# Kernel tuning notes

Hardware: AMD Instinct MI355X
Metric: run time of the kernel (lower is better)

The kernel has to match this reference:

```python
import jax, jax.numpy as jnp
import numpy as np

B, H, S, D = 1, 16, 4096, 64


def setup_inputs() -> dict:
    key = jax.random.key(0)
    kq, kk, kv = jax.random.split(key, 3)
    Q = jax.random.normal(kq, (B, H, S, D), dtype=jnp.float32)
    K = jax.random.normal(kk, (B, H, S, D), dtype=jnp.float32)
    V = jax.random.normal(kv, (B, H, S, D), dtype=jnp.float32)
    # causal mask, broadcast over batch/heads: True = attend
    mask = jnp.tril(jnp.ones((S, S), dtype=bool))[None, None, :, :]
    return {"Q": Q, "K": K, "V": V, "mask": mask}


def reference(Q, K, V, mask):
    d_k = Q.shape[-1]
    scale = 1.0 / jnp.sqrt(jnp.asarray(d_k, dtype=Q.dtype))
    # [..., q, k] scores; mask==False positions set to -inf before softmax
    scores = jnp.einsum('...qd,...kd->...qk', Q, K) * scale
    scores = jnp.where(mask, scores, jnp.asarray(-jnp.inf, dtype=scores.dtype))
    attn = jax.nn.softmax(scores, axis=-1)
    return jnp.einsum('...qk,...kd->...qd', attn, V)
```

## Files before the change

### kernel.cpp

```cpp
#include <hip/hip_runtime.h>
#include <hip/hip_bf16.h>

typedef __attribute__((ext_vector_type(8))) short short8;
typedef __attribute__((ext_vector_type(4))) short s4v;
typedef __attribute__((ext_vector_type(2))) int   int2v;
typedef __attribute__((ext_vector_type(4))) float floatx4;

#define MFMA16(A,B,C) __builtin_amdgcn_mfma_f32_16x16x32_bf16(A,B,C,0,0,0)
#define LDS_FENCE() asm volatile("s_waitcnt lgkmcnt(0)" ::: "memory")

__device__ __forceinline__ short bf16bits(float x) {
    __hip_bfloat16 h = __float2bfloat16(x);
    return *(short*)&h;
}
__device__ __forceinline__ short8 cvt8(const float* p) {
    floatx4 a = *(const floatx4*)p;
    floatx4 b = *(const floatx4*)(p + 4);
    short8 r;
    r[0]=bf16bits(a.x); r[1]=bf16bits(a.y); r[2]=bf16bits(a.z); r[3]=bf16bits(a.w);
    r[4]=bf16bits(b.x); r[5]=bf16bits(b.y); r[6]=bf16bits(b.z); r[7]=bf16bits(b.w);
    return r;
}
__device__ __forceinline__ short8 cvt8s(const float* p) {
    constexpr float SCL2 = 0.125f * 1.44269504088896f;
    floatx4 a = *(const floatx4*)p;
    floatx4 b = *(const floatx4*)(p + 4);
    a *= SCL2; b *= SCL2;
    short8 r;
    r[0]=bf16bits(a.x); r[1]=bf16bits(a.y); r[2]=bf16bits(a.z); r[3]=bf16bits(a.w);
    r[4]=bf16bits(b.x); r[5]=bf16bits(b.y); r[6]=bf16bits(b.z); r[7]=bf16bits(b.w);
    return r;
}
__device__ __forceinline__ int pk2(float lo, float hi) {
    int r;
    asm("v_cvt_pk_bf16_f32 %0, %1, %2" : "=v"(r) : "v"(lo), "v"(hi));
    return r;
}

__global__ __launch_bounds__(256) void prep(const float* __restrict__ V,
                                            short* __restrict__ VT,
                                            const float* __restrict__ K,
                                            short* __restrict__ K16, int doK)
{
    __shared__ short tile[64 * 65];
    const int t  = threadIdx.x;
    const int h  = blockIdx.x >> 6;
    const int s0 = (blockIdx.x & 63) << 6;
    const float* src = V + ((size_t)h * 4096 + s0) * 64;
    const int r = t >> 4, dq = (t & 15) * 4;
#pragma unroll
    for (int pass = 0; pass < 4; ++pass) {
        const int s = pass * 16 + r;
        floatx4 f = *(const floatx4*)(src + s * 64 + dq);
        short* w = tile + s * 65 + dq;
        w[0] = bf16bits(f.x); w[1] = bf16bits(f.y);
        w[2] = bf16bits(f.z); w[3] = bf16bits(f.w);
    }
    __syncthreads();
    const int d = t >> 2, sc = (t & 3) * 16;
    short8 a, b;
#pragma unroll
    for (int j = 0; j < 8; ++j) a[j] = tile[(sc + j) * 65 + d];
#pragma unroll
    for (int j = 0; j < 8; ++j) b[j] = tile[(sc + 8 + j) * 65 + d];
    short* dst = VT + ((size_t)h * 64 + d) * 4096 + s0 + sc;
    *(short8*)dst       = a;
    *(short8*)(dst + 8) = b;
    if (doK) {
        const size_t base = (size_t)blockIdx.x * 4096 + (size_t)t * 16;
        *(short8*)(K16 + base)     = cvt8(K + base);
        *(short8*)(K16 + base + 8) = cvt8(K + base + 8);
    }
}

template<bool KB16>
__global__ __launch_bounds__(256, 4)
void attn_fast(const float* __restrict__ Qg, const float* __restrict__ Kg,
               const short* __restrict__ K16g, const short* __restrict__ VTg,
               float* __restrict__ Og)
{
    constexpr int S = 4096, D = 64;

    __shared__ __align__(16) short lK[4096];
    __shared__ __align__(16) short lV[4096];
    __shared__ __align__(16) short lP[4096];

    const int tid = threadIdx.x;
    const int wv  = tid >> 6;
    const int ln  = tid & 63;
    const int ll  = ln & 15;
    const int qd  = ln >> 4;

    const int c = blockIdx.x & 255;
    const int s = blockIdx.x >> 8;
    const int h = c & 15;
    const int x = c >> 4;
    const int qblk = (s == 0) ? (63 - x) : (s == 1) ? (32 + x) : (s == 2) ? (31 - x) : x;
    const int qb   = qblk << 6;
    const int qrow = qb + wv * 16;

    const float* Qh  = Qg  + (size_t)h * S * D;
    const float* Kf  = Kg  + (size_t)h * S * D;
    const short* K16 = K16g + (size_t)h * S * D;
    const short* Vt  = VTg + (size_t)h * 64 * S;

    short8 qf0, qf1;
    {
        const float* qp = Qh + (qrow + ll) * D + qd * 8;
        qf0 = cvt8s(qp);
        qf1 = cvt8s(qp + 32);
    }

    floatx4 o[4], ol;
#pragma unroll
    for (int dt = 0; dt < 4; ++dt) o[dt] = (floatx4){0.f, 0.f, 0.f, 0.f};
    ol = (floatx4){0.f, 0.f, 0.f, 0.f};

    short8 ones;
#pragma unroll
    for (int j = 0; j < 8; ++j) ones[j] = (short)0x3F80;

    const int kkey = tid >> 3, kd8 = tid & 7;
    const int koct = kd8 & 3;
    short* kdst = lK + ((kkey >> 4) * 2 + (kd8 >> 2)) * 512
                     + ((((kkey & 15) | (koct << 4)) ^ (koct * 5)) * 8);
    const float* ksrcf = Kf  + kkey * 64 + kd8 * 8;
    const short* ksrc6 = K16 + kkey * 64 + kd8 * 8;
    const int vd = tid >> 2, voct = tid & 3;
    short* vdst = lV + (vd >> 4) * 512
                     + ((((vd & 15) | (voct << 4)) ^ (voct * 5)) * 8);
    const short* vsrc = Vt + (size_t)vd * S + voct * 8;
    const int rblk = ((ll | (qd << 4)) ^ (qd * 5));
    const int pswz  = (ll >> 1) & 3;
    short* lPw = lP + wv * 1024;
    const int pw0 = ll * 32 + (((qd >> 1) ^ pswz) * 8) + (qd & 1) * 4;
    const int prd = ll * 32 + ((qd ^ pswz) * 8);

    const int kv_end = qb + 64;
    const int wv_end = qrow + 16;

    auto ldK = [&](int kv) -> short8 {
        return KB16 ? *(const short8*)(ksrc6 + kv * 64) : cvt8(ksrcf + kv * 64);
    };

    short8 kpre0 = ldK(0),  kpre1 = ldK(32);
    short8 vpre0 = *(const short8*)(vsrc);
    short8 vpre1 = *(const short8*)(vsrc + 32);

    for (int kv = 0; kv < kv_end; kv += 64) {
        __syncthreads();
        *(short8*)kdst          = kpre0;
        *(short8*)(kdst + 2048) = kpre1;
        *(short8*)vdst          = vpre0;
        *(short8*)(vdst + 2048) = vpre1;
        __syncthreads();
        if (kv + 64 < kv_end) {
            kpre0 = ldK(kv + 64);
            kpre1 = ldK(kv + 96);
            vpre0 = *(const short8*)(vsrc + kv + 64);
            vpre1 = *(const short8*)(vsrc + kv + 96);
        }

        if (kv < wv_end) {
            const bool h1 = (kv + 32 < wv_end);
            floatx4 sc0 = (floatx4){0.f, 0.f, 0.f, 0.f};
            floatx4 sc1 = sc0, sc2 = sc0, sc3 = sc0;
            short8 kf;
            __builtin_amdgcn_s_setprio(1);
            kf = ((const short8*)(lK +    0))[rblk]; sc0 = MFMA16(kf, qf0, sc0);
            kf = ((const short8*)(lK +  512))[rblk]; sc0 = MFMA16(kf, qf1, sc0);
            kf = ((const short8*)(lK + 1024))[rblk]; sc1 = MFMA16(kf, qf0, sc1);
            kf = ((const short8*)(lK + 1536))[rblk]; sc1 = MFMA16(kf, qf1, sc1);
            if (h1) {
                kf = ((const short8*)(lK + 2048))[rblk]; sc2 = MFMA16(kf, qf0, sc2);
                kf = ((const short8*)(lK + 2560))[rblk]; sc2 = MFMA16(kf, qf1, sc2);
                kf = ((const short8*)(lK + 3072))[rblk]; sc3 = MFMA16(kf, qf0, sc3);
                kf = ((const short8*)(lK + 3584))[rblk]; sc3 = MFMA16(kf, qf1, sc3);
            }
            __builtin_amdgcn_s_setprio(0);

            float p0[4], p1[4];
#pragma unroll
            for (int r = 0; r < 4; ++r) {
                p0[r] = exp2f(sc0[r]);
                p1[r] = exp2f(sc1[r]);
            }
            if (kv + 31 > qrow) {
                const int qg = qrow + ll;
                const int k0 = kv + qd * 4, k1 = k0 + 16;
#pragma unroll
                for (int r = 0; r < 4; ++r) {
                    if (k0 + r > qg) p0[r] = 0.f;
                    if (k1 + r > qg) p1[r] = 0.f;
                }
            }
            *(int2v*)(lPw + pw0)        = (int2v){pk2(p0[0],p0[1]), pk2(p0[2],p0[3])};
            *(int2v*)(lPw + (pw0 ^ 16)) = (int2v){pk2(p1[0],p1[1]), pk2(p1[2],p1[3])};
            if (h1) {
                float p2[4], p3[4];
#pragma unroll
                for (int r = 0; r < 4; ++r) {
                    p2[r] = exp2f(sc2[r]);
                    p3[r] = exp2f(sc3[r]);
                }
                if (kv + 63 > qrow) {
                    const int qg = qrow + ll;
                    const int k2 = kv + 32 + qd * 4, k3 = k2 + 16;
#pragma unroll
                    for (int r = 0; r < 4; ++r) {
                        if (k2 + r > qg) p2[r] = 0.f;
                        if (k3 + r > qg) p3[r] = 0.f;
                    }
                }
                *(int2v*)(lPw + 512 + pw0)        = (int2v){pk2(p2[0],p2[1]), pk2(p2[2],p2[3])};
                *(int2v*)(lPw + 512 + (pw0 ^ 16)) = (int2v){pk2(p3[0],p3[1]), pk2(p3[2],p3[3])};
            }
            LDS_FENCE();
            short8 pf0 = *(const short8*)(lPw + prd);
            __builtin_amdgcn_s_setprio(1);
#pragma unroll
            for (int dt = 0; dt < 4; ++dt) {
                short8 vf = ((const short8*)(lV + dt * 512))[rblk];
                o[dt] = MFMA16(pf0, vf, o[dt]);
            }
            ol = MFMA16(pf0, ones, ol);
            if (h1) {
                short8 pf1 = *(const short8*)(lPw + 512 + prd);
#pragma unroll
                for (int dt = 0; dt < 4; ++dt) {
                    short8 vf = ((const short8*)(lV + 2048 + dt * 512))[rblk];
                    o[dt] = MFMA16(pf1, vf, o[dt]);
                }
                ol = MFMA16(pf1, ones, ol);
            }
            __builtin_amdgcn_s_setprio(0);
        }
    }

#pragma unroll
    for (int r = 0; r < 4; ++r) {
        const float rl = 1.f / fmaxf(ol[r], 1e-37f);
        const int q = qrow + qd * 4 + r;
        float* op = Og + ((size_t)h * S + q) * D + ll;
#pragma unroll
        for (int dt = 0; dt < 4; ++dt)
            op[dt * 16] = o[dt][r] * rl;
    }
}

__global__ __launch_bounds__(256, 4)
void attn_legacy(const float* __restrict__ Qg, const float* __restrict__ Kg,
                 const float* __restrict__ Vg, float* __restrict__ Og)
{
    constexpr int S = 4096, D = 64;
    constexpr float SCL2 = 0.125f * 1.44269504088896f;
    constexpr float NEG  = -1.0e30f;
    __shared__ __align__(16) short lK[2048];
    __shared__ __align__(16) short lV[2048];
    __shared__ __align__(16) short lP[2048];
    const int tid = threadIdx.x, wv = tid >> 6, ln = tid & 63, ll = ln & 15, qd = ln >> 4;
    const int bid = blockIdx.x, h = bid & 15, qblk = 63 - (bid >> 4), qb = qblk << 6;
    const float* Qh = Qg + (size_t)h * S * D;
    const float* Kh = Kg + (size_t)h * S * D;
    const float* Vh = Vg + (size_t)h * S * D;
    const int qrow = qb + wv * 16;
    short8 qf0, qf1;
    { const float* qp = Qh + (qrow + ll) * D + qd * 8; qf0 = cvt8(qp); qf1 = cvt8(qp + 32); }
    floatx4 o[4]; float mi[4], li[4];
#pragma unroll
    for (int dt = 0; dt < 4; ++dt) o[dt] = (floatx4){0.f,0.f,0.f,0.f};
#pragma unroll
    for (int r = 0; r < 4; ++r) { mi[r] = NEG; li[r] = 0.f; }
    const int k_st = tid >> 3, dbase = (tid & 7) * 8;
    const int sq = (dbase >> 3) & 3, sks = dbase >> 5;
    const int kw_slot = (((k_st >> 4) * 2 + sks) * 64)
                      + (((sq << 4) | (k_st & 15)) ^ (sq | (sks << 2)));
    const int kr0 = ln ^ qd, kr1 = ln ^ (qd | 4), vbit3 = (ln >> 3) & 1;
    const int kv_end = qb + 64, wv_end = qrow + 16;
    for (int kv = 0; kv < kv_end; kv += 32) {
        __syncthreads();
        {
            short8 kval = cvt8(Kh + (kv + k_st) * D + dbase);
            ((short8*)lK)[kw_slot] = kval;
            short8 vval = cvt8(Vh + (kv + k_st) * D + dbase);
            const int vq = (k_st >> 3) << 4, vj = k_st & 7;
#pragma unroll
            for (int i = 0; i < 8; ++i) {
                int d = dbase + i, dt = d >> 4, l2 = d & 15;
                int lp = (vq | l2) ^ (((l2 >> 3) & 1) | (dt << 1));
                lV[dt * 512 + lp * 8 + vj] = vval[i];
            }
        }
        __syncthreads();
        if (kv < wv_end) {
            floatx4 sc0 = (floatx4){0.f,0.f,0.f,0.f}, sc1 = sc0; short8 kf;
            kf = ((const short8*)lK)[0*64+kr0]; sc0 = MFMA16(qf0, kf, sc0);
            kf = ((const short8*)lK)[1*64+kr1]; sc0 = MFMA16(qf1, kf, sc0);
            kf = ((const short8*)lK)[2*64+kr0]; sc1 = MFMA16(qf0, kf, sc1);
            kf = ((const short8*)lK)[3*64+kr1]; sc1 = MFMA16(qf1, kf, sc1);
            float p0[4], p1[4]; const int qg = qrow + qd * 4;
#pragma unroll
            for (int r = 0; r < 4; ++r) { p0[r] = sc0[r]*SCL2; p1[r] = sc1[r]*SCL2; }
            if (kv + 31 > qrow) {
                const int k0 = kv + ll, k1 = kv + 16 + ll;
#pragma unroll
                for (int r = 0; r < 4; ++r) {
                    if (k0 > qg + r) p0[r] = NEG;
                    if (k1 > qg + r) p1[r] = NEG;
                }
            }
#pragma unroll
            for (int r = 0; r < 4; ++r) {
                float mx = fmaxf(p0[r], p1[r]);
                mx = fmaxf(mx, __shfl_xor(mx,1)); mx = fmaxf(mx, __shfl_xor(mx,2));
                mx = fmaxf(mx, __shfl_xor(mx,4)); mx = fmaxf(mx, __shfl_xor(mx,8));
                const float nm = fmaxf(mi[r], mx);
                const float a = exp2f(mi[r] - nm); mi[r] = nm;
                p0[r] = exp2f(p0[r] - nm); p1[r] = exp2f(p1[r] - nm);
                float ps = p0[r] + p1[r];
                ps += __shfl_xor(ps,1); ps += __shfl_xor(ps,2);
                ps += __shfl_xor(ps,4); ps += __shfl_xor(ps,8);
                li[r] = li[r] * a + ps;
#pragma unroll
                for (int dt = 0; dt < 4; ++dt) o[dt][r] *= a;
            }
            {
                const int pbase = wv * 512 + (ll & 7);
                const int dl0 = ((ll >> 3) << 4) + qd * 4;
#pragma unroll
                for (int r = 0; r < 4; ++r) {
                    lP[pbase + (dl0 + r) * 8]      = bf16bits(p0[r]);
                    lP[pbase + (dl0 + 32 + r) * 8] = bf16bits(p1[r]);
                }
            }
            __threadfence_block();
            short8 pf = ((const short8*)lP)[wv * 64 + ln];
#pragma unroll
            for (int dt = 0; dt < 4; ++dt) {
                short8 vf = ((const short8*)lV)[dt * 64 + (ln ^ (vbit3 | (dt << 1)))];
                o[dt] = MFMA16(pf, vf, o[dt]);
            }
        }
    }
#pragma unroll
    for (int r = 0; r < 4; ++r) {
        const float rl = 1.f / fmaxf(li[r], 1e-30f);
        const int q = qrow + qd * 4 + r;
        float* op = Og + ((size_t)h * S + q) * D + ll;
#pragma unroll
        for (int dt = 0; dt < 4; ++dt) op[dt * 16] = o[dt][r] * rl;
    }
}

extern "C" void kernel_launch(void* const* d_in, const int* in_sizes, int n_in,
                              void* d_out, int out_size, void* d_ws, size_t ws_size,
                              hipStream_t stream) {
    const float* Q = (const float*)d_in[0];
    const float* K = (const float*)d_in[1];
    const float* V = (const float*)d_in[2];
    float* O = (float*)d_out;
    const size_t elems  = (size_t)16 * 4096 * 64;
    const size_t oneBuf = elems * sizeof(short);
    if (ws_size >= 2 * oneBuf) {
        short* VT  = (short*)d_ws;
        short* K16 = (short*)d_ws + elems;
        prep<<<dim3(1024), dim3(256), 0, stream>>>(V, VT, K, K16, 1);
        attn_fast<true><<<dim3(1024), dim3(256), 0, stream>>>(Q, K, K16, VT, O);
    } else if (ws_size >= oneBuf) {
        short* VT = (short*)d_ws;
        prep<<<dim3(1024), dim3(256), 0, stream>>>(V, VT, K, VT, 0);
        attn_fast<false><<<dim3(1024), dim3(256), 0, stream>>>(Q, K, nullptr, VT, O);
    } else {
        attn_legacy<<<dim3(1024), dim3(256), 0, stream>>>(Q, K, V, O);
    }
}
```

Measured before the change: 197.7 us.

## Double query rows per wave to reuse K/V LDS fragments across two tiles

Each wave now handles 32 query rows (two 16-row MFMA tiles) instead of 16, so every K and V fragment read from LDS feeds two MFMAs. Blocks cover 128 queries, the grid halves to 512 blocks, and the causal scheduling pairs blocks as (31-x, x) to balance work. The P buffer doubles and launch bounds drop to 2 blocks per CU to leave room for the extra registers. The cost is lower occupancy, fewer blocks to spread across CUs, and more wasted masked work on diagonal tiles.

After: 223.8 us. 1.13x slower.

```diff
diff --git a/kernel.cpp b/kernel.cpp
--- a/kernel.cpp
+++ b/kernel.cpp
@@ -74,7 +74,7 @@
 }
 
 template<bool KB16>
-__global__ __launch_bounds__(256, 4)
+__global__ __launch_bounds__(256, 2)
 void attn_fast(const float* __restrict__ Qg, const float* __restrict__ Kg,
                const short* __restrict__ K16g, const short* __restrict__ VTg,
                float* __restrict__ Og)
@@ -83,7 +83,7 @@
 
     __shared__ __align__(16) short lK[4096];
     __shared__ __align__(16) short lV[4096];
-    __shared__ __align__(16) short lP[4096];
+    __shared__ __align__(16) short lP[8192];
 
     const int tid = threadIdx.x;
     const int wv  = tid >> 6;
@@ -95,26 +95,28 @@
     const int s = blockIdx.x >> 8;
     const int h = c & 15;
     const int x = c >> 4;
-    const int qblk = (s == 0) ? (63 - x) : (s == 1) ? (32 + x) : (s == 2) ? (31 - x) : x;
-    const int qb   = qblk << 6;
-    const int qrow = qb + wv * 16;
+    const int qblk = (s == 0) ? (31 - x) : x;
+    const int qb   = qblk << 7;
+    const int qrow = qb + wv * 32;
 
     const float* Qh  = Qg  + (size_t)h * S * D;
     const float* Kf  = Kg  + (size_t)h * S * D;
     const short* K16 = K16g + (size_t)h * S * D;
     const short* Vt  = VTg + (size_t)h * 64 * S;
 
-    short8 qf0, qf1;
+    short8 qA0, qA1, qB0, qB1;
     {
         const float* qp = Qh + (qrow + ll) * D + qd * 8;
-        qf0 = cvt8s(qp);
-        qf1 = cvt8s(qp + 32);
-    }
-
-    floatx4 o[4], ol;
-#pragma unroll
-    for (int dt = 0; dt < 4; ++dt) o[dt] = (floatx4){0.f, 0.f, 0.f, 0.f};
-    ol = (floatx4){0.f, 0.f, 0.f, 0.f};
+        qA0 = cvt8s(qp);       qA1 = cvt8s(qp + 32);
+        const float* qp2 = qp + 16 * D;
+        qB0 = cvt8s(qp2);      qB1 = cvt8s(qp2 + 32);
+    }
+
+    floatx4 oA[4], oB[4], olA, olB;
+#pragma unroll
+    for (int dt = 0; dt < 4; ++dt) { oA[dt] = (floatx4){0.f,0.f,0.f,0.f}; oB[dt] = oA[dt]; }
+    olA = (floatx4){0.f,0.f,0.f,0.f};
+    olB = olA;
 
     short8 ones;
 #pragma unroll
@@ -132,12 +134,12 @@
     const short* vsrc = Vt + (size_t)vd * S + voct * 8;
     const int rblk = ((ll | (qd << 4)) ^ (qd * 5));
     const int pswz  = (ll >> 1) & 3;
-    short* lPw = lP + wv * 1024;
+    short* lPw = lP + wv * 2048;
     const int pw0 = ll * 32 + (((qd >> 1) ^ pswz) * 8) + (qd & 1) * 4;
     const int prd = ll * 32 + ((qd ^ pswz) * 8);
 
-    const int kv_end = qb + 64;
-    const int wv_end = qrow + 16;
+    const int kv_end = qb + 128;
+    const int wv_end = qrow + 32;
 
     auto ldK = [&](int kv) -> short8 {
         return KB16 ? *(const short8*)(ksrc6 + kv * 64) : cvt8(ksrcf + kv * 64);
@@ -146,6 +148,23 @@
     short8 kpre0 = ldK(0),  kpre1 = ldK(32);
     short8 vpre0 = *(const short8*)(vsrc);
     short8 vpre1 = *(const short8*)(vsrc + 32);
+
+#define SOFTMAX_STORE(S0, S1, QG, BASE, KVH) do {                              \
+    float p0_[4], p1_[4];                                                      \
+    _Pragma("unroll")                                                          \
+    for (int r = 0; r < 4; ++r) { p0_[r] = exp2f((S0)[r]); p1_[r] = exp2f((S1)[r]); } \
+    if ((KVH) + 31 > (QG)) {                                                   \
+        const int qg_ = (QG) + ll;                                             \
+        const int k0_ = (KVH) + qd * 4, k1_ = k0_ + 16;                        \
+        _Pragma("unroll")                                                      \
+        for (int r = 0; r < 4; ++r) {                                          \
+            if (k0_ + r > qg_) p0_[r] = 0.f;                                   \
+            if (k1_ + r > qg_) p1_[r] = 0.f;                                   \
+        }                                                                      \
+    }                                                                          \
+    *(int2v*)((BASE) + pw0)        = (int2v){pk2(p0_[0],p0_[1]), pk2(p0_[2],p0_[3])}; \
+    *(int2v*)((BASE) + (pw0 ^ 16)) = (int2v){pk2(p1_[0],p1_[1]), pk2(p1_[2],p1_[3])}; \
+} while (0)
 
     for (int kv = 0; kv < kv_end; kv += 64) {
         __syncthreads();
@@ -163,88 +182,78 @@
 
         if (kv < wv_end) {
             const bool h1 = (kv + 32 < wv_end);
-            floatx4 sc0 = (floatx4){0.f, 0.f, 0.f, 0.f};
-            floatx4 sc1 = sc0, sc2 = sc0, sc3 = sc0;
+            floatx4 zz = (floatx4){0.f,0.f,0.f,0.f};
+            floatx4 sA0=zz, sA1=zz, sA2=zz, sA3=zz;
+            floatx4 sB0=zz, sB1=zz, sB2=zz, sB3=zz;
             short8 kf;
             __builtin_amdgcn_s_setprio(1);
-            kf = ((const short8*)(lK +    0))[rblk]; sc0 = MFMA16(kf, qf0, sc0);
-            kf = ((const short8*)(lK +  512))[rblk]; sc0 = MFMA16(kf, qf1, sc0);
-            kf = ((const short8*)(lK + 1024))[rblk]; sc1 = MFMA16(kf, qf0, sc1);
-            kf = ((const short8*)(lK + 1536))[rblk]; sc1 = MFMA16(kf, qf1, sc1);
+            kf = ((const short8*)(lK +    0))[rblk]; sA0 = MFMA16(kf, qA0, sA0); sB0 = MFMA16(kf, qB0, sB0);
+            kf = ((const short8*)(lK +  512))[rblk]; sA0 = MFMA16(kf, qA1, sA0); sB0 = MFMA16(kf, qB1, sB0);
+            kf = ((const short8*)(lK + 1024))[rblk]; sA1 = MFMA16(kf, qA0, sA1); sB1 = MFMA16(kf, qB0, sB1);
+            kf = ((const short8*)(lK + 1536))[rblk]; sA1 = MFMA16(kf, qA1, sA1); sB1 = MFMA16(kf, qB1, sB1);
             if (h1) {
-                kf = ((const short8*)(lK + 2048))[rblk]; sc2 = MFMA16(kf, qf0, sc2);
-                kf = ((const short8*)(lK + 2560))[rblk]; sc2 = MFMA16(kf, qf1, sc2);
-                kf = ((const short8*)(lK + 3072))[rblk]; sc3 = MFMA16(kf, qf0, sc3);
-                kf = ((const short8*)(lK + 3584))[rblk]; sc3 = MFMA16(kf, qf1, sc3);
+                kf = ((const short8*)(lK + 2048))[rblk]; sA2 = MFMA16(kf, qA0, sA2); sB2 = MFMA16(kf, qB0, sB2);
+                kf = ((const short8*)(lK + 2560))[rblk]; sA2 = MFMA16(kf, qA1, sA2); sB2 = MFMA16(kf, qB1, sB2);
+                kf = ((const short8*)(lK + 3072))[rblk]; sA3 = MFMA16(kf, qA0, sA3); sB3 = MFMA16(kf, qB0, sB3);
+                kf = ((const short8*)(lK + 3584))[rblk]; sA3 = MFMA16(kf, qA1, sA3); sB3 = MFMA16(kf, qB1, sB3);
             }
             __builtin_amdgcn_s_setprio(0);
 
-            float p0[4], p1[4];
-#pragma unroll
-            for (int r = 0; r < 4; ++r) {
-                p0[r] = exp2f(sc0[r]);
-                p1[r] = exp2f(sc1[r]);
-            }
-            if (kv + 31 > qrow) {
-                const int qg = qrow + ll;
-                const int k0 = kv + qd * 4, k1 = k0 + 16;
-#pragma unroll
-                for (int r = 0; r < 4; ++r) {
-                    if (k0 + r > qg) p0[r] = 0.f;
-                    if (k1 + r > qg) p1[r] = 0.f;
-                }
-            }
-            *(int2v*)(lPw + pw0)        = (int2v){pk2(p0[0],p0[1]), pk2(p0[2],p0[3])};
-            *(int2v*)(lPw + (pw0 ^ 16)) = (int2v){pk2(p1[0],p1[1]), pk2(p1[2],p1[3])};
+            SOFTMAX_STORE(sA0, sA1, qrow,      lPw,        kv);
+            SOFTMAX_STORE(sB0, sB1, qrow + 16, lPw + 1024, kv);
             if (h1) {
-                float p2[4], p3[4];
-#pragma unroll
-                for (int r = 0; r < 4; ++r) {
-                    p2[r] = exp2f(sc2[r]);
-                    p3[r] = exp2f(sc3[r]);
-                }
-                if (kv + 63 > qrow) {
-                    const int qg = qrow + ll;
-                    const int k2 = kv + 32 + qd * 4, k3 = k2 + 16;
-#pragma unroll
-                    for (int r = 0; r < 4; ++r) {
-                        if (k2 + r > qg) p2[r] = 0.f;
-                        if (k3 + r > qg) p3[r] = 0.f;
-                    }
-                }
-                *(int2v*)(lPw + 512 + pw0)        = (int2v){pk2(p2[0],p2[1]), pk2(p2[2],p2[3])};
-                *(int2v*)(lPw + 512 + (pw0 ^ 16)) = (int2v){pk2(p3[0],p3[1]), pk2(p3[2],p3[3])};
+                SOFTMAX_STORE(sA2, sA3, qrow,      lPw + 512,  kv + 32);
+                SOFTMAX_STORE(sB2, sB3, qrow + 16, lPw + 1536, kv + 32);
             }
             LDS_FENCE();
-            short8 pf0 = *(const short8*)(lPw + prd);
+
+            short8 pfA = *(const short8*)(lPw + prd);
+            short8 pfB = *(const short8*)(lPw + 1024 + prd);
             __builtin_amdgcn_s_setprio(1);
 #pragma unroll
             for (int dt = 0; dt < 4; ++dt) {
                 short8 vf = ((const short8*)(lV + dt * 512))[rblk];
-                o[dt] = MFMA16(pf0, vf, o[dt]);
-            }
-            ol = MFMA16(pf0, ones, ol);
+                oA[dt] = MFMA16(pfA, vf, oA[dt]);
+                oB[dt] = MFMA16(pfB, vf, oB[dt]);
+            }
+            olA = MFMA16(pfA, ones, olA);
+            olB = MFMA16(pfB, ones, olB);
+            __builtin_amdgcn_s_setprio(0);
             if (h1) {
-                short8 pf1 = *(const short8*)(lPw + 512 + prd);
+                short8 pfA1 = *(const short8*)(lPw + 512 + prd);
+                short8 pfB1 = *(const short8*)(lPw + 1536 + prd);
+                __builtin_amdgcn_s_setprio(1);
 #pragma unroll
                 for (int dt = 0; dt < 4; ++dt) {
                     short8 vf = ((const short8*)(lV + 2048 + dt * 512))[rblk];
-                    o[dt] = MFMA16(pf1, vf, o[dt]);
+                    oA[dt] = MFMA16(pfA1, vf, oA[dt]);
+                    oB[dt] = MFMA16(pfB1, vf, oB[dt]);
                 }
-                ol = MFMA16(pf1, ones, ol);
-            }
-            __builtin_amdgcn_s_setprio(0);
+                olA = MFMA16(pfA1, ones, olA);
+                olB = MFMA16(pfB1, ones, olB);
+                __builtin_amdgcn_s_setprio(0);
+            }
         }
     }
+#undef SOFTMAX_STORE
 
 #pragma unroll
     for (int r = 0; r < 4; ++r) {
-        const float rl = 1.f / fmaxf(ol[r], 1e-37f);
+        const float rl = 1.f / fmaxf(olA[r], 1e-37f);
         const int q = qrow + qd * 4 + r;
         float* op = Og + ((size_t)h * S + q) * D + ll;
 #pragma unroll
         for (int dt = 0; dt < 4; ++dt)
-            op[dt * 16] = o[dt][r] * rl;
+            op[dt * 16] = oA[dt][r] * rl;
+    }
+#pragma unroll
+    for (int r = 0; r < 4; ++r) {
+        const float rl = 1.f / fmaxf(olB[r], 1e-37f);
+        const int q = qrow + 16 + qd * 4 + r;
+        float* op = Og + ((size_t)h * S + q) * D + ll;
+#pragma unroll
+        for (int dt = 0; dt < 4; ++dt)
+            op[dt * 16] = oB[dt][r] * rl;
     }
 }
 
@@ -365,11 +374,11 @@
         short* VT  = (short*)d_ws;
         short* K16 = (short*)d_ws + elems;
         prep<<<dim3(1024), dim3(256), 0, stream>>>(V, VT, K, K16, 1);
-        attn_fast<true><<<dim3(1024), dim3(256), 0, stream>>>(Q, K, K16, VT, O);
+        attn_fast<true><<<dim3(512), dim3(256), 0, stream>>>(Q, K, K16, VT, O);
     } else if (ws_size >= oneBuf) {
         short* VT = (short*)d_ws;
         prep<<<dim3(1024), dim3(256), 0, stream>>>(V, VT, K, VT, 0);
-        attn_fast<false><<<dim3(1024), dim3(256), 0, stream>>>(Q, K, nullptr, VT, O);
+        attn_fast<false><<<dim3(512), dim3(256), 0, stream>>>(Q, K, nullptr, VT, O);
     } else {
         attn_legacy<<<dim3(1024), dim3(256), 0, stream>>>(Q, K, V, O);
     }
```
